# Kernel optimization log

Measured on AMD Instinct MI355X. Metric: run time of the kernel, lower is better.

The kernel has to match this reference:

```python
import jax, jax.numpy as jnp
import numpy as np

HIDDEN = 768
N_HEADS = 12
D_HEAD = 64
B, T = 4, 2048


def setup_inputs() -> dict:
    key = jax.random.key(0)
    ks = jax.random.split(key, 5)
    s = 0.02
    return {
        "x": jax.random.normal(ks[0], (B, T, HIDDEN), dtype=jnp.float32),
        "w_q": jax.random.normal(ks[1], (HIDDEN, HIDDEN), dtype=jnp.float32) * s,
        "w_k": jax.random.normal(ks[2], (HIDDEN, HIDDEN), dtype=jnp.float32) * s,
        "w_v": jax.random.normal(ks[3], (HIDDEN, HIDDEN), dtype=jnp.float32) * s,
        "w_o": jax.random.normal(ks[4], (HIDDEN, HIDDEN), dtype=jnp.float32) * s,
    }


def reference(x, w_q, w_k, w_v, w_o):
    # nn.Linear applies x @ W^T; weights here are [out, in] like torch.
    b, t, h = x.shape
    q = (x @ w_q.T).reshape(b, t, N_HEADS, D_HEAD)
    k = (x @ w_k.T).reshape(b, t, N_HEADS, D_HEAD)
    v = (x @ w_v.T).reshape(b, t, N_HEADS, D_HEAD)
    # scores: [b, heads, t, t]
    scores = jnp.einsum("bqhd,bkhd->bhqk", q, k) / jnp.sqrt(jnp.float32(D_HEAD))
    weights = jax.nn.softmax(scores, axis=-1)
    # dropout p=0.0 -> identity
    ctx = jnp.einsum("bhqk,bkhd->bqhd", weights, v).reshape(b, t, h)
    return ctx @ w_o.T
```

## Files before the change

kernel.cpp:

```cpp
#include <hip/hip_runtime.h>

#define HIDDEN 768
#define NH 12
#define DH 64
#define BB 4
#define TT 2048
#define MTOT (BB * TT)

typedef __bf16 bf16x8 __attribute__((ext_vector_type(8)));
typedef short s16x8 __attribute__((ext_vector_type(8)));
typedef float f32x4 __attribute__((ext_vector_type(4)));

__device__ __forceinline__ unsigned short f2b(float f) {
    unsigned u = __builtin_bit_cast(unsigned, f);
    u += 0x7fffu + ((u >> 16) & 1u);
    return (unsigned short)(u >> 16);
}

__device__ __forceinline__ unsigned pack_bf16(float a, float b) {
    return __builtin_amdgcn_perm(__builtin_bit_cast(unsigned, b),
                                 __builtin_bit_cast(unsigned, a), 0x07060302u);
}

typedef const __attribute__((address_space(1))) unsigned int* gas_ptr;
typedef __attribute__((address_space(3))) unsigned int* las_ptr;
__device__ __forceinline__ void gload16(const void* g, void* l) {
    __builtin_amdgcn_global_load_lds((gas_ptr)(uintptr_t)g, (las_ptr)(uintptr_t)l, 16, 0, 0);
}

__global__ __launch_bounds__(256) void cvt_all(const float* __restrict__ x,
                                               const float* __restrict__ wq,
                                               const float* __restrict__ wk,
                                               const float* __restrict__ wv,
                                               const float* __restrict__ wo,
                                               unsigned short* __restrict__ out) {
    const size_t NX8 = (size_t)MTOT * HIDDEN / 8;
    const size_t NW8 = (size_t)HIDDEN * HIDDEN / 8;
    size_t i = (size_t)blockIdx.x * 256 + threadIdx.x;
    const float* src;
    size_t off = i;
    float scale = 1.0f;
    if (i < NX8) { src = x; }
    else if (i < NX8 + NW8) { src = wq; off = i - NX8; scale = 0.18033688011112042f; }
    else if (i < NX8 + 2 * NW8) { src = wk; off = i - NX8 - NW8; }
    else if (i < NX8 + 3 * NW8) { src = wv; off = i - NX8 - 2 * NW8; }
    else { src = wo; off = i - NX8 - 3 * NW8; }
    const float4* p = (const float4*)src + off * 2;
    float4 a = p[0], b = p[1];
    union { uint4 u; unsigned short s[8]; } t;
    t.s[0] = f2b(a.x * scale); t.s[1] = f2b(a.y * scale);
    t.s[2] = f2b(a.z * scale); t.s[3] = f2b(a.w * scale);
    t.s[4] = f2b(b.x * scale); t.s[5] = f2b(b.y * scale);
    t.s[6] = f2b(b.z * scale); t.s[7] = f2b(b.w * scale);
    ((uint4*)out)[i] = t.u;
}

template <int MODE, int MROWS>
__device__ __forceinline__ void gemm_body(const unsigned short* __restrict__ A,
                                          const unsigned short* __restrict__ Bm,
                                          float* __restrict__ Cf,
                                          unsigned short* __restrict__ Cb,
                                          int mBase, int nBase, int N) {
    __shared__ __align__(16) unsigned short Al[MROWS][64];
    __shared__ __align__(16) unsigned short Bl[128][64];
    const int MT = MROWS / 32;
    const int tid = threadIdx.x;
    const int lane = tid & 63;
    const int wave = tid >> 6;
    const int quad = lane >> 4;
    const int l16 = lane & 15;
    const int mw = (wave >> 1) * (MROWS / 2);
    const int nw = (wave & 1) * 64;
    const int r8 = lane >> 3;
    const int swiz = ((lane & 7) ^ r8) * 8;
    const unsigned short* Asrc = A + (size_t)(mBase + wave * (MROWS / 4) + r8) * HIDDEN + swiz;
    const unsigned short* Bsrc = Bm + (size_t)(nBase + wave * 32 + r8) * HIDDEN + swiz;

    f32x4 acc[MT][4];
#pragma unroll
    for (int mt = 0; mt < MT; ++mt)
#pragma unroll
        for (int nt = 0; nt < 4; ++nt) acc[mt][nt] = (f32x4){0.f, 0.f, 0.f, 0.f};

    for (int kb = 0; kb < HIDDEN / 64; ++kb) {
        if (kb) __syncthreads();
#pragma unroll
        for (int i = 0; i < MROWS / 32; ++i)
            gload16(Asrc + (size_t)i * 8 * HIDDEN + kb * 64,
                    &Al[wave * (MROWS / 4) + i * 8][0]);
#pragma unroll
        for (int j = 0; j < 4; ++j)
            gload16(Bsrc + (size_t)j * 8 * HIDDEN + kb * 64, &Bl[wave * 32 + j * 8][0]);
        __syncthreads();
#pragma unroll
        for (int ks = 0; ks < 2; ++ks) {
            const int cc = ((ks * 4 + quad) ^ (l16 & 7)) * 8;
            bf16x8 af[MT], bf[4];
#pragma unroll
            for (int mt = 0; mt < MT; ++mt)
                af[mt] = *(const bf16x8*)&Al[mw + mt * 16 + l16][cc];
#pragma unroll
            for (int nt = 0; nt < 4; ++nt)
                bf[nt] = *(const bf16x8*)&Bl[nw + nt * 16 + l16][cc];
#pragma unroll
            for (int mt = 0; mt < MT; ++mt)
#pragma unroll
                for (int nt = 0; nt < 4; ++nt)
                    acc[mt][nt] = __builtin_amdgcn_mfma_f32_16x16x32_bf16(
                        af[mt], bf[nt], acc[mt][nt], 0, 0, 0);
        }
    }

#pragma unroll
    for (int mt = 0; mt < MT; ++mt)
#pragma unroll
        for (int nt = 0; nt < 4; ++nt) {
            if (MODE == 2) {
                ushort4 h;
                h.x = f2b(acc[mt][nt][0]); h.y = f2b(acc[mt][nt][1]);
                h.z = f2b(acc[mt][nt][2]); h.w = f2b(acc[mt][nt][3]);
                int m0 = mBase + mw + mt * 16 + quad * 4;
                int col = nBase + nw + nt * 16 + l16;
                *(ushort4*)&Cb[(size_t)col * MTOT + m0] = h;
            } else {
#pragma unroll
                for (int r = 0; r < 4; ++r) {
                    int row = mBase + mw + mt * 16 + quad * 4 + r;
                    int col = nBase + nw + nt * 16 + l16;
                    float v = acc[mt][nt][r];
                    if (MODE == 1)
                        Cf[(size_t)row * N + col] = v;
                    else
                        Cb[(size_t)row * N + col] = f2b(v);
                }
            }
        }
}

__global__ __launch_bounds__(256, 4) void gemm_qkv(const unsigned short* __restrict__ A,
                                                   const unsigned short* __restrict__ W0,
                                                   unsigned short* __restrict__ C0,
                                                   unsigned short* __restrict__ VT) {
    const int wsel = blockIdx.y / 6;
    const int nb = blockIdx.y % 6;
    if (wsel < 2)
        gemm_body<0, 128>(A, W0 + (size_t)wsel * HIDDEN * HIDDEN, nullptr,
                          C0 + (size_t)wsel * MTOT * HIDDEN, blockIdx.x * 128, nb * 128, HIDDEN);
    else
        gemm_body<2, 128>(A, W0 + 2 * (size_t)HIDDEN * HIDDEN, nullptr, VT,
                          blockIdx.x * 128, nb * 128, HIDDEN);
}

__global__ __launch_bounds__(256, 4) void gemm_out(const unsigned short* __restrict__ A,
                                                   const unsigned short* __restrict__ Bm,
                                                   float* __restrict__ Cf) {
    gemm_body<1, 128>(A, Bm, Cf, nullptr, blockIdx.x * 128, blockIdx.y * 128, HIDDEN);
}

__global__ __launch_bounds__(256, 3) void attn_kernel(const unsigned short* __restrict__ Qg,
                                                      const unsigned short* __restrict__ Kg,
                                                      const unsigned short* __restrict__ VTg,
                                                      unsigned short* __restrict__ Ctx) {
    __shared__ __align__(16) unsigned short Kl[2][64][64];
    __shared__ __align__(16) unsigned short Vl[2][64][64];
    __shared__ __align__(16) unsigned int Pl[4][32][32];
    const int tid = threadIdx.x;
    const int lane = tid & 63;
    const int wave = tid >> 6;
    const int quad = lane >> 4;
    const int l16 = lane & 15;
    const int qt = blockIdx.y;
    const int bh = blockIdx.x;
    const int b = bh / NH, h = bh % NH;
    const int qrow0 = b * TT + qt * 128;
    const int col0 = h * DH;

    const int srow = wave * 16 + (lane >> 3);
    const int swiz = ((lane & 7) ^ (lane >> 3)) * 8;
    const unsigned short* Ksrc = Kg + (size_t)(b * TT + srow) * HIDDEN + col0 + swiz;
    const unsigned short* Vsrc = VTg + (size_t)(col0 + srow) * MTOT + b * TT + swiz;

    auto stage = [&](int buf, int kt) {
#pragma unroll
        for (int i = 0; i < 2; ++i) {
            gload16(Ksrc + (size_t)(kt * 64 + i * 8) * HIDDEN, &Kl[buf][wave * 16 + i * 8][0]);
            gload16(Vsrc + (size_t)(i * 8) * MTOT + kt * 64, &Vl[buf][wave * 16 + i * 8][0]);
        }
    };

    bf16x8 qf[2][2];
#pragma unroll
    for (int mt = 0; mt < 2; ++mt)
#pragma unroll
        for (int ks = 0; ks < 2; ++ks)
            qf[mt][ks] = *(const bf16x8*)&Qg[(size_t)(qrow0 + wave * 32 + mt * 16 + l16) * HIDDEN +
                                             col0 + ks * 32 + quad * 8];

    s16x8 osv;
#pragma unroll
    for (int e = 0; e < 8; ++e) osv[e] = 0x3F80;
    const bf16x8 ones = __builtin_bit_cast(bf16x8, osv);

    f32x4 o[2][4];
    f32x4 lacc[2];
#pragma unroll
    for (int mt = 0; mt < 2; ++mt) {
        lacc[mt] = (f32x4){0.f, 0.f, 0.f, 0.f};
#pragma unroll
        for (int nt = 0; nt < 4; ++nt) o[mt][nt] = (f32x4){0.f, 0.f, 0.f, 0.f};
    }

    const int rx = l16 & 7;
    const f32x4 z4 = (f32x4){0.f, 0.f, 0.f, 0.f};

    stage(0, 0);
    for (int kt = 0; kt < TT / 64; ++kt) {
        __syncthreads();
        if (kt + 1 < TT / 64) stage((kt + 1) & 1, kt + 1);
        const int buf = kt & 1;

        f32x4 s[2][4];
#pragma unroll
        for (int ks = 0; ks < 2; ++ks) {
            const int cc = ((ks * 4 + quad) ^ rx) * 8;
            bf16x8 kf[4];
#pragma unroll
            for (int nt = 0; nt < 4; ++nt)
                kf[nt] = *(const bf16x8*)&Kl[buf][nt * 16 + l16][cc];
            __builtin_amdgcn_s_setprio(1);
#pragma unroll
            for (int mt = 0; mt < 2; ++mt)
#pragma unroll
                for (int nt = 0; nt < 4; ++nt)
                    s[mt][nt] = __builtin_amdgcn_mfma_f32_16x16x32_bf16(
                        kf[nt], qf[mt][ks], ks ? s[mt][nt] : z4, 0, 0, 0);
            __builtin_amdgcn_s_setprio(0);
        }

#pragma unroll
        for (int mt = 0; mt < 2; ++mt) {
            const int row = mt * 16 + l16;
#pragma unroll
            for (int nt = 0; nt < 4; ++nt) {
                float p0 = __builtin_amdgcn_exp2f(s[mt][nt][0]);
                float p1 = __builtin_amdgcn_exp2f(s[mt][nt][1]);
                float p2 = __builtin_amdgcn_exp2f(s[mt][nt][2]);
                float p3 = __builtin_amdgcn_exp2f(s[mt][nt][3]);
                uint2 w;
                w.x = pack_bf16(p0, p1);
                w.y = pack_bf16(p2, p3);
                const int unit = 2 * nt + (quad >> 1);
                *(uint2*)&Pl[wave][row][(((unit ^ rx) << 2) | ((quad & 1) << 1))] = w;
            }
        }

#pragma unroll
        for (int ks = 0; ks < 2; ++ks) {
            const int cc = ((ks * 4 + quad) ^ rx) * 8;
            bf16x8 pf[2], vf[4];
#pragma unroll
            for (int mt = 0; mt < 2; ++mt)
                pf[mt] = *(const bf16x8*)((const char*)&Pl[wave][mt * 16 + l16][0] +
                                          ((((ks * 4 + quad) ^ rx) << 4)));
#pragma unroll
            for (int nt = 0; nt < 4; ++nt)
                vf[nt] = *(const bf16x8*)&Vl[buf][nt * 16 + l16][cc];
            __builtin_amdgcn_s_setprio(1);
#pragma unroll
            for (int mt = 0; mt < 2; ++mt)
                lacc[mt] = __builtin_amdgcn_mfma_f32_16x16x32_bf16(pf[mt], ones, lacc[mt], 0, 0, 0);
#pragma unroll
            for (int mt = 0; mt < 2; ++mt)
#pragma unroll
                for (int nt = 0; nt < 4; ++nt)
                    o[mt][nt] = __builtin_amdgcn_mfma_f32_16x16x32_bf16(pf[mt], vf[nt],
                                                                        o[mt][nt], 0, 0, 0);
            __builtin_amdgcn_s_setprio(0);
        }
    }

#pragma unroll
    for (int mt = 0; mt < 2; ++mt)
#pragma unroll
        for (int r = 0; r < 4; ++r) {
            float inv = __builtin_amdgcn_rcpf(lacc[mt][r]);
            int row = qrow0 + wave * 32 + mt * 16 + quad * 4 + r;
#pragma unroll
            for (int nt = 0; nt < 4; ++nt)
                Ctx[(size_t)row * HIDDEN + col0 + nt * 16 + l16] = f2b(o[mt][nt][r] * inv);
        }
}

extern "C" void kernel_launch(void* const* d_in, const int* in_sizes, int n_in,
                              void* d_out, int out_size, void* d_ws, size_t ws_size,
                              hipStream_t stream) {
    const float* x = (const float*)d_in[0];
    const float* wq = (const float*)d_in[1];
    const float* wk = (const float*)d_in[2];
    const float* wv = (const float*)d_in[3];
    const float* wo = (const float*)d_in[4];
    float* out = (float*)d_out;

    const size_t NX = (size_t)MTOT * HIDDEN;
    const size_t NW = (size_t)HIDDEN * HIDDEN;
    unsigned short* ws = (unsigned short*)d_ws;
    unsigned short* xb = ws;
    unsigned short* wqb = xb + NX;
    unsigned short* wob = wqb + 3 * NW;
    unsigned short* qb = wob + NW;
    unsigned short* kb = qb + NX;
    unsigned short* cb = kb + NX;
    unsigned short* vtb = cb + NX;

    cvt_all<<<(int)((NX + 4 * NW) / 8 / 256), 256, 0, stream>>>(x, wq, wk, wv, wo, xb);

    gemm_qkv<<<dim3(MTOT / 128, 18), 256, 0, stream>>>(xb, wqb, qb, vtb);

    attn_kernel<<<dim3(BB * NH, TT / 128), 256, 0, stream>>>(qb, kb, vtb, cb);

    gemm_out<<<dim3(MTOT / 128, 6), 256, 0, stream>>>(cb, wob, out);
}
```

Baseline: 198.8 us.

## Fuse Q/K/V projections into one GEMM tile sharing the A tile

Replaces the generic per-weight QKV GEMM with a dedicated kernel in which each block loads one 64-row tile of x and multiplies it against the matching 128-column slices of all three weight matrices. The A tile is reused across Q, K and V, so activation reads from memory drop to a third. The cost is 96 accumulator registers per lane and an occupancy hint lowered from 4 to 2 blocks. The tiles are smaller (64 rows, 768 blocks in place of 1152), with no double buffering, so latency hiding may suffer.

```diff
diff --git a/kernel.cpp b/kernel.cpp
--- a/kernel.cpp
+++ b/kernel.cpp
@@ -137,18 +137,97 @@
         }
 }
 
-__global__ __launch_bounds__(256, 4) void gemm_qkv(const unsigned short* __restrict__ A,
+__global__ __launch_bounds__(256, 2) void gemm_qkv(const unsigned short* __restrict__ A,
                                                    const unsigned short* __restrict__ W0,
                                                    unsigned short* __restrict__ C0,
                                                    unsigned short* __restrict__ VT) {
-    const int wsel = blockIdx.y / 6;
-    const int nb = blockIdx.y % 6;
-    if (wsel < 2)
-        gemm_body<0, 128>(A, W0 + (size_t)wsel * HIDDEN * HIDDEN, nullptr,
-                          C0 + (size_t)wsel * MTOT * HIDDEN, blockIdx.x * 128, nb * 128, HIDDEN);
-    else
-        gemm_body<2, 128>(A, W0 + 2 * (size_t)HIDDEN * HIDDEN, nullptr, VT,
-                          blockIdx.x * 128, nb * 128, HIDDEN);
+    __shared__ __align__(16) unsigned short Al[64][64];
+    __shared__ __align__(16) unsigned short Bl[3][128][64];
+    const size_t NWW = (size_t)HIDDEN * HIDDEN;
+    const size_t NX = (size_t)MTOT * HIDDEN;
+    const int tid = threadIdx.x;
+    const int lane = tid & 63;
+    const int wave = tid >> 6;
+    const int quad = lane >> 4;
+    const int l16 = lane & 15;
+    const int rx = l16 & 7;
+    const int mw = (wave >> 1) * 32;
+    const int nw = (wave & 1) * 64;
+    const int r8 = lane >> 3;
+    const int swiz = ((lane & 7) ^ r8) * 8;
+    const int mBase = blockIdx.x * 64;
+    const int nBase = blockIdx.y * 128;
+    const unsigned short* Asrc = A + (size_t)(mBase + wave * 16 + r8) * HIDDEN + swiz;
+    const unsigned short* Bsrc = W0 + (size_t)(nBase + wave * 32 + r8) * HIDDEN + swiz;
+
+    f32x4 acc[3][2][4];
+#pragma unroll
+    for (int w = 0; w < 3; ++w)
+#pragma unroll
+        for (int mt = 0; mt < 2; ++mt)
+#pragma unroll
+            for (int nt = 0; nt < 4; ++nt) acc[w][mt][nt] = (f32x4){0.f, 0.f, 0.f, 0.f};
+
+    for (int kb = 0; kb < HIDDEN / 64; ++kb) {
+        if (kb) __syncthreads();
+#pragma unroll
+        for (int i = 0; i < 2; ++i)
+            gload16(Asrc + (size_t)i * 8 * HIDDEN + kb * 64, &Al[wave * 16 + i * 8][0]);
+#pragma unroll
+        for (int w = 0; w < 3; ++w)
+#pragma unroll
+            for (int j = 0; j < 4; ++j)
+                gload16(Bsrc + (size_t)w * NWW + (size_t)j * 8 * HIDDEN + kb * 64,
+                        &Bl[w][wave * 32 + j * 8][0]);
+        __syncthreads();
+#pragma unroll
+        for (int ks = 0; ks < 2; ++ks) {
+            const int cc = ((ks * 4 + quad) ^ rx) * 8;
+            bf16x8 af[2];
+#pragma unroll
+            for (int mt = 0; mt < 2; ++mt)
+                af[mt] = *(const bf16x8*)&Al[mw + mt * 16 + l16][cc];
+#pragma unroll
+            for (int w = 0; w < 3; ++w) {
+                bf16x8 bf[4];
+#pragma unroll
+                for (int nt = 0; nt < 4; ++nt)
+                    bf[nt] = *(const bf16x8*)&Bl[w][nw + nt * 16 + l16][cc];
+                __builtin_amdgcn_s_setprio(1);
+#pragma unroll
+                for (int mt = 0; mt < 2; ++mt)
+#pragma unroll
+                    for (int nt = 0; nt < 4; ++nt)
+                        acc[w][mt][nt] = __builtin_amdgcn_mfma_f32_16x16x32_bf16(
+                            af[mt], bf[nt], acc[w][mt][nt], 0, 0, 0);
+                __builtin_amdgcn_s_setprio(0);
+            }
+        }
+    }
+
+#pragma unroll
+    for (int w = 0; w < 3; ++w)
+#pragma unroll
+        for (int mt = 0; mt < 2; ++mt)
+#pragma unroll
+            for (int nt = 0; nt < 4; ++nt) {
+                if (w == 2) {
+                    ushort4 h;
+                    h.x = f2b(acc[2][mt][nt][0]); h.y = f2b(acc[2][mt][nt][1]);
+                    h.z = f2b(acc[2][mt][nt][2]); h.w = f2b(acc[2][mt][nt][3]);
+                    int m0 = mBase + mw + mt * 16 + quad * 4;
+                    int col = nBase + nw + nt * 16 + l16;
+                    *(ushort4*)&VT[(size_t)col * MTOT + m0] = h;
+                } else {
+                    unsigned short* Cb = C0 + (size_t)w * NX;
+#pragma unroll
+                    for (int r = 0; r < 4; ++r) {
+                        int row = mBase + mw + mt * 16 + quad * 4 + r;
+                        int col = nBase + nw + nt * 16 + l16;
+                        Cb[(size_t)row * HIDDEN + col] = f2b(acc[w][mt][nt][r]);
+                    }
+                }
+            }
 }
 
 __global__ __launch_bounds__(256, 4) void gemm_out(const unsigned short* __restrict__ A,
@@ -314,7 +393,7 @@
 
     cvt_all<<<(int)((NX + 4 * NW) / 8 / 256), 256, 0, stream>>>(x, wq, wk, wv, wo, xb);
 
-    gemm_qkv<<<dim3(MTOT / 128, 18), 256, 0, stream>>>(xb, wqb, qb, vtb);
+    gemm_qkv<<<dim3(MTOT / 64, 6), 256, 0, stream>>>(xb, wqb, qb, vtb);
 
     attn_kernel<<<dim3(BB * NH, TT / 128), 256, 0, stream>>>(qb, kb, vtb, cb);
 
```

Measured after the change: 198.9 us. About the same (+0.1%).
